# Optimization experiments

Measured on AMD Instinct MI355X. Metric: run time of the kernel, lower is better.

The kernel has to match this reference:

```python
import jax, jax.numpy as jnp
import numpy as np
from jax import lax

V, E, F, TL, NS, B = 10000, 150, 200, 7, 4, 2048
PAD_IDX = 1
EPS = 1e-5
SLOPE = 0.01  # nn.LeakyReLU default


def leaky(x):
    return jnp.where(x >= 0, x, SLOPE * x)


def conv1d(x, w, b):
    # x [B,Cin,L], w [Cout,Cin,K] -> [B,Cout,L-K+1]
    y = lax.conv_general_dilated(x, w, (1,), 'VALID',
                                 dimension_numbers=('NCH', 'OIH', 'NCH'))
    return y + b[None, :, None]


def batchnorm(x, g, b):
    # training-mode BatchNorm1d over [B,C,L]: stats over (B,L), biased var
    m = jnp.mean(x, axis=(0, 2), keepdims=True)
    v = jnp.mean((x - m) ** 2, axis=(0, 2), keepdims=True)
    return (x - m) * lax.rsqrt(v + EPS) * g[None, :, None] + b[None, :, None]


def setup_inputs() -> dict:
    key = jax.random.key(0)
    ks = jax.random.split(key, 24)
    s = 0.05
    inp = {
        'text': jax.random.randint(ks[0], (NS * TL, B), 0, V, dtype=jnp.int32).astype(jnp.int64) if False else jax.random.randint(ks[0], (NS * TL, B), 0, V),
        'ith_sentence': 4,
        'idx': 1,
        'emb': jax.random.normal(ks[1], (V, E), jnp.float32) * s,
        'gamma': jnp.ones((F,), jnp.float32),
        'beta': jnp.zeros((F,), jnp.float32),
        'conv1_w': jax.random.normal(ks[2], (F, E, 2), jnp.float32) * s,
        'conv1_b': jax.random.normal(ks[3], (F,), jnp.float32) * s,
        'conv2_w': jax.random.normal(ks[4], (F, F, 2), jnp.float32) * s,
        'conv2_b': jax.random.normal(ks[5], (F,), jnp.float32) * s,
        'conv3_w': jax.random.normal(ks[6], (F, F, 3), jnp.float32) * s,
        'conv3_b': jax.random.normal(ks[7], (F,), jnp.float32) * s,
        'conv4_w': jax.random.normal(ks[8], (F, F, 3), jnp.float32) * s,
        'conv4_b': jax.random.normal(ks[9], (F,), jnp.float32) * s,
        'M_w': jax.random.normal(ks[10], (F, 2 * F), jnp.float32) * s,
        'M_b': jax.random.normal(ks[11], (F,), jnp.float32) * s,
        'U_w': jax.random.normal(ks[12], (7, F, F), jnp.float32) * s,
        'U_b': jax.random.normal(ks[13], (7, F), jnp.float32) * s,
        'R_w': jax.random.normal(ks[14], (F, F), jnp.float32) * s,
        'R_b': jax.random.normal(ks[15], (F,), jnp.float32) * s,
        'H_w': jax.random.normal(ks[16], (F, F), jnp.float32) * s,
        'H_b': jax.random.normal(ks[17], (F,), jnp.float32) * s,
        'X_w': jax.random.normal(ks[18], (F, V), jnp.float32) * s,
        'X_b': jax.random.normal(ks[19], (F,), jnp.float32) * s,
        'Y_w': jax.random.normal(ks[20], (V, F), jnp.float32) * s,
        'Y_b': jax.random.normal(ks[21], (V,), jnp.float32) * s,
    }
    return inp


def _forward(text, ith_sentence, emb, gamma, beta,
             conv1_w, conv1_b, conv2_w, conv2_b, conv3_w, conv3_b,
             conv4_w, conv4_b, M_w, M_b, U_w, U_b, R_w, R_b,
             H_w, H_b, X_w, X_b, Y_w, Y_b):
    batch = text.shape[1]
    embedded = jnp.transpose(emb[text], (1, 2, 0))  # [B,E,S]

    # conv encoder per preceding sentence (Python loop over fixed small count)
    vecs = []
    for j in range(1, ith_sentence):
        seg = embedded[:, :, (j - 1) * TL: j * TL]        # [B,E,7]
        o = leaky(batchnorm(conv1d(seg, conv1_w, conv1_b), gamma, beta))  # L=6
        o = leaky(batchnorm(conv1d(o, conv2_w, conv2_b), gamma, beta))    # L=5
        o = leaky(batchnorm(conv1d(o, conv3_w, conv3_b), gamma, beta))    # L=3
        o = leaky(conv1d(o, conv4_w, conv4_b))                            # L=1
        vecs.append(o[:, :, 0])                           # [B,F]

    h = jnp.zeros((batch, F), embedded.dtype)
    for i in range(ith_sentence - 1):
        h = leaky(jnp.concatenate([vecs[i], h], axis=1) @ M_w.T + M_b)

    # u vectors; faithfully reproduce the original's u1-overwrite in the
    # text_len==7 branch: u1 becomes relu(U7(h)); u6,u7 stay un-activated.
    Uh = jnp.einsum('bf,tgf->tbg', h, U_w) + U_b[:, None, :]  # [7,B,F]
    Ur = leaky(Uh)
    u_steps = jnp.stack([Ur[6], Ur[1], Ur[2], Ur[3], Ur[4], Uh[5], Uh[6]])

    h_terms = jnp.einsum('tbf,gf->tbg', u_steps, H_w) + H_b   # [7,B,F]
    targets = lax.dynamic_slice_in_dim(text, (ith_sentence - 1) * TL, TL, 0)  # [7,B]

    XwT = X_w.T  # [V,F]; X(onehot(w)) == XwT[w] + X_b (same math, direct gather)

    def step(carry, xs):
        r, w = carry
        h_term, tgt = xs
        r = leaky(r @ R_w.T + R_b + XwT[w] + X_b + h_term)    # [B,F]
        y = r @ Y_w.T + Y_b                                   # [B,V]
        logp = jax.nn.log_softmax(y, axis=-1)
        loss_t = -jnp.mean(jnp.take_along_axis(logp, tgt[:, None], 1)[:, 0])
        pred = jnp.argmax(y, axis=1)
        correct_t = jnp.sum((pred == tgt).astype(jnp.int32))
        return (r, pred), (loss_t, correct_t)

    w0 = jnp.zeros((batch,), targets.dtype)
    r0 = jnp.zeros((batch, F), h.dtype)
    _, (losses, corrects) = lax.scan(step, (r0, w0), (h_terms, targets))
    return jnp.sum(losses), jnp.sum(corrects)


def reference(text, ith_sentence, idx, emb, gamma, beta,
              conv1_w, conv1_b, conv2_w, conv2_b, conv3_w, conv3_b,
              conv4_w, conv4_b, M_w, M_b, U_w, U_b, R_w, R_b,
              H_w, H_b, X_w, X_b, Y_w, Y_b):
    loss, correct = _forward(text, int(ith_sentence), emb, gamma, beta,
                             conv1_w, conv1_b, conv2_w, conv2_b,
                             conv3_w, conv3_b, conv4_w, conv4_b,
                             M_w, M_b, U_w, U_b, R_w, R_b,
                             H_w, H_b, X_w, X_b, Y_w, Y_b)
    return loss, correct
```

## Files before the change

### kernel.cpp

```cpp
#include <hip/hip_runtime.h>
#include <math.h>

#define V_    10000
#define VP_   10048
#define E_    150
#define F_    200
#define TL_   7
#define B_    2048
#define NSEG_ 3
#define EPS_  1e-5f
#define SLOPE_ 0.01f
#define NB64  (B_/64)
#define NVB   157
#define NYB   1280
#define KQ_   7

typedef unsigned short u16;
typedef __attribute__((ext_vector_type(8))) short bf16x8;
typedef __attribute__((ext_vector_type(4))) float f32x4;

#define SB0() __builtin_amdgcn_sched_barrier(0)

__device__ __forceinline__ float leaky_f(float x){ return x >= 0.f ? x : SLOPE_*x; }
__device__ __forceinline__ u16 bf16_rne(float x){
  unsigned u = __float_as_uint(x);
  unsigned r = (u + 0x7FFFu + ((u>>16)&1u)) >> 16;
  return (u16)r;
}
__device__ __forceinline__ float bf16_to_f(u16 h){ return __uint_as_float(((unsigned)h)<<16); }

__global__ void transpose_k(const float* __restrict__ in, float* __restrict__ out,
                            int R, int C)
{
  __shared__ float tile[32][33];
  const long long bofs = (long long)blockIdx.z * R * C;
  in += bofs; out += bofs;
  const int c0 = blockIdx.x*32, r0 = blockIdx.y*32;
  const int tx = threadIdx.x, ty = threadIdx.y;
  for (int i = ty; i < 32; i += 8) {
    int r = r0 + i, c = c0 + tx;
    if (r < R && c < C) tile[i][tx] = in[(long long)r*C + c];
  }
  __syncthreads();
  for (int i = ty; i < 32; i += 8) {
    int c = c0 + i, r = r0 + tx;
    if (c < C && r < R) out[(long long)c*R + r] = tile[tx][i];
  }
}

__global__ void gather_x0(const int* __restrict__ text, const float* __restrict__ emb,
                          float* __restrict__ X0)
{
  const int b = blockIdx.x*256 + threadIdx.x;
  const int l = blockIdx.y, j = blockIdx.z;
  const int s = j*TL_ + l;
  const int row = text[(long long)s*B_ + b];
  const float* er = emb + (long long)row*E_;
  float* xp = X0 + ((long long)j*E_*TL_ + l)*B_ + b;
  for (int e = 0; e < E_; ++e) xp[(long long)e*TL_*B_] = er[e];
}

struct PWEnt { const float* src; u16* dh; u16* dl; int kstride; int keff; int nq; };
struct PWTab { PWEnt e[14]; };

__global__ void pack_all_w(PWTab tab)
{
  const PWEnt E = tab.e[blockIdx.y];
  const int q = blockIdx.x;
  if (q >= E.nq) return;
  const int f = threadIdx.x;
  union { u16 u[32]; uint4 v[4]; } H, L;
  #pragma unroll
  for (int kk = 0; kk < 32; ++kk) {
    const int k = q*32 + kk;
    const float x = (k < E.keff && f < F_) ? E.src[(size_t)f*E.kstride + k] : 0.f;
    const u16 h = bf16_rne(x);
    H.u[kk] = h;
    L.u[kk] = bf16_rne(x - bf16_to_f(h));
  }
  uint4* dh = (uint4*)(E.dh + ((size_t)q*256 + f)*32);
  uint4* dl = (uint4*)(E.dl + ((size_t)q*256 + f)*32);
  #pragma unroll
  for (int i = 0; i < 4; ++i) { dh[i] = H.v[i]; dl[i] = L.v[i]; }
}

__global__ void pack_x(const float* __restrict__ X, long long xZ,
                       u16* __restrict__ Oh, u16* __restrict__ Ol, long long oZ)
{
  const int q = blockIdx.y, z = blockIdx.z;
  const int b = blockIdx.x*256 + threadIdx.x;
  X  += (size_t)z*xZ;
  Oh += (size_t)z*oZ; Ol += (size_t)z*oZ;
  union { u16 u[32]; uint4 v[4]; } H, L;
  #pragma unroll
  for (int kk = 0; kk < 32; ++kk) {
    const int k = q*32 + kk;
    const float x = (k < F_) ? X[(size_t)k*B_ + b] : 0.f;
    const u16 h = bf16_rne(x);
    H.u[kk] = h;
    L.u[kk] = bf16_rne(x - bf16_to_f(h));
  }
  uint4* dh = (uint4*)(Oh + ((size_t)q*B_ + b)*32);
  uint4* dl = (uint4*)(Ol + ((size_t)q*B_ + b)*32);
  #pragma unroll
  for (int i = 0; i < 4; ++i) { dh[i] = H.v[i]; dl[i] = L.v[i]; }
}

__global__ void us_pack(const float* __restrict__ Uh,
                        u16* __restrict__ Oh, u16* __restrict__ Ol, long long oZ)
{
  const int q = blockIdx.y, t = blockIdx.z;
  const int b = blockIdx.x*256 + threadIdx.x;
  const int src = (t == 0) ? 6 : t;
  const float* U = Uh + (size_t)src*F_*B_;
  Oh += (size_t)t*oZ; Ol += (size_t)t*oZ;
  union { u16 u[32]; uint4 v[4]; } H, L;
  #pragma unroll
  for (int kk = 0; kk < 32; ++kk) {
    const int k = q*32 + kk;
    float x = 0.f;
    if (k < F_) {
      x = U[(size_t)k*B_ + b];
      if (t < 5) x = leaky_f(x);
    }
    const u16 h = bf16_rne(x);
    H.u[kk] = h;
    L.u[kk] = bf16_rne(x - bf16_to_f(h));
  }
  uint4* dh = (uint4*)(Oh + ((size_t)q*B_ + b)*32);
  uint4* dl = (uint4*)(Ol + ((size_t)q*B_ + b)*32);
  #pragma unroll
  for (int i = 0; i < 4; ++i) { dh[i] = H.v[i]; dl[i] = L.v[i]; }
}

struct MFrag { bf16x8 h1[4], l1[4], h2[4], l2[4]; };

template<bool TWO>
__device__ __forceinline__ void m_loadq(MFrag& f, int q,
    const u16* __restrict__ X1h, const u16* __restrict__ X1l,
    const u16* __restrict__ X2h, const u16* __restrict__ X2l,
    int b0, int lr, int g)
{
  #pragma unroll
  for (int nt = 0; nt < 4; ++nt) {
    const size_t o = ((size_t)q*B_ + (b0 + nt*16 + lr))*32 + g*8;
    f.h1[nt] = *(const bf16x8*)(X1h + o);
    f.l1[nt] = *(const bf16x8*)(X1l + o);
    if (TWO) {
      f.h2[nt] = *(const bf16x8*)(X2h + o);
      f.l2[nt] = *(const bf16x8*)(X2l + o);
    }
  }
}

template<bool TWO>
__device__ __forceinline__ void m_mfma_chunk(const MFrag& f, int q,
    const u16* __restrict__ W1h, const u16* __restrict__ W1l,
    const u16* __restrict__ W2h, const u16* __restrict__ W2l,
    int f0, int w, int lr, int g, f32x4 acc[4])
{
  const size_t aoff = ((size_t)q*256 + (f0 + w*16 + lr))*32 + g*8;
  {
    const bf16x8 ah = *(const bf16x8*)(W1h + aoff);
    const bf16x8 al = *(const bf16x8*)(W1l + aoff);
    #pragma unroll
    for (int nt = 0; nt < 4; ++nt) {
      acc[nt] = __builtin_amdgcn_mfma_f32_16x16x32_bf16(ah, f.h1[nt], acc[nt], 0, 0, 0);
      acc[nt] = __builtin_amdgcn_mfma_f32_16x16x32_bf16(ah, f.l1[nt], acc[nt], 0, 0, 0);
      acc[nt] = __builtin_amdgcn_mfma_f32_16x16x32_bf16(al, f.h1[nt], acc[nt], 0, 0, 0);
    }
  }
  if (TWO) {
    const bf16x8 ah = *(const bf16x8*)(W2h + aoff);
    const bf16x8 al = *(const bf16x8*)(W2l + aoff);
    #pragma unroll
    for (int nt = 0; nt < 4; ++nt) {
      acc[nt] = __builtin_amdgcn_mfma_f32_16x16x32_bf16(ah, f.h2[nt], acc[nt], 0, 0, 0);
      acc[nt] = __builtin_amdgcn_mfma_f32_16x16x32_bf16(ah, f.l2[nt], acc[nt], 0, 0, 0);
      acc[nt] = __builtin_amdgcn_mfma_f32_16x16x32_bf16(al, f.h2[nt], acc[nt], 0, 0, 0);
    }
  }
}

template<bool TWO, bool LEAKY, bool OUT_F32, bool OUT_PK>
__global__ __launch_bounds__(256) void mf_gemm(
    const u16* __restrict__ W1h, const u16* __restrict__ W1l, long long wZ,
    const u16* __restrict__ X1h, const u16* __restrict__ X1l, long long xZ,
    const u16* __restrict__ W2h, const u16* __restrict__ W2l,
    const u16* __restrict__ X2h, const u16* __restrict__ X2l,
    const float* __restrict__ bias, long long bZ,
    float* __restrict__ Cf, long long cZ,
    u16* __restrict__ Oh, u16* __restrict__ Ol)
{
  const int z = blockIdx.z;
  W1h += (size_t)z*wZ; W1l += (size_t)z*wZ;
  X1h += (size_t)z*xZ; X1l += (size_t)z*xZ;
  const float* bz = bias + (size_t)z*bZ;
  if (OUT_F32) Cf += (size_t)z*cZ;

  const int f0 = blockIdx.x*64;
  const int b0 = blockIdx.y*64;
  const int tid = threadIdx.x;
  const int w = tid >> 6, l = tid & 63;
  const int lr = l & 15, g = l >> 4;

  __shared__ float T[64][65];

  f32x4 acc[4] = {};
  MFrag fA, fB;
  m_loadq<TWO>(fA, 0, X1h, X1l, X2h, X2l, b0, lr, g);
  #pragma unroll
  for (int q = 0; q < KQ_; ++q) {
    MFrag& cur = (q & 1) ? fB : fA;
    MFrag& nxt = (q & 1) ? fA : fB;
    if (q + 1 < KQ_) m_loadq<TWO>(nxt, q + 1, X1h, X1l, X2h, X2l, b0, lr, g);
    SB0();
    m_mfma_chunk<TWO>(cur, q, W1h, W1l, W2h, W2l, f0, w, lr, g, acc);
    SB0();
  }
  #pragma unroll
  for (int nt = 0; nt < 4; ++nt)
    #pragma unroll
    for (int j = 0; j < 4; ++j)
      T[w*16 + g*4 + j][nt*16 + lr] = acc[nt][j];
  __syncthreads();

  const int ty = tid >> 4, tx = tid & 15;
  #pragma unroll
  for (int i = 0; i < 4; ++i) {
    const int f = f0 + ty*4 + i;
    if (f < F_) {
      const float bb = bz[f];
      #pragma unroll
      for (int j = 0; j < 4; ++j) {
        float v = T[ty*4 + i][tx*4 + j] + bb;
        if (LEAKY) v = leaky_f(v);
        if (OUT_F32) Cf[(size_t)f*B_ + b0 + tx*4 + j] = v;
        T[ty*4 + i][tx*4 + j] = v;
      }
    } else {
      #pragma unroll
      for (int j = 0; j < 4; ++j) T[ty*4 + i][tx*4 + j] = 0.f;
    }
  }
  __syncthreads();

  if (OUT_PK) {
    const int bcol = tid & 63;
    const int kk0 = (tid >> 6)*8;
    #pragma unroll
    for (int qh = 0; qh < 2; ++qh) {
      const int q = (f0 >> 5) + qh;
      if (q >= KQ_) continue;
      union { u16 u[8]; uint4 v2[1]; } H, L;
      #pragma unroll
      for (int u = 0; u < 8; ++u) {
        const float x = T[qh*32 + kk0 + u][bcol];
        const u16 h = bf16_rne(x);
        H.u[u] = h;
        L.u[u] = bf16_rne(x - bf16_to_f(h));
      }
      const size_t off = ((size_t)q*B_ + b0 + bcol)*32 + kk0;
      *(uint4*)(Oh + off) = H.v2[0];
      *(uint4*)(Ol + off) = L.v2[0];
    }
  }
}

struct CFrag { bf16x8 bh[4], bl[4]; };

__device__ __forceinline__ void c_mfma_chunk(const CFrag& f, int q,
    const u16* __restrict__ Wh, const u16* __restrict__ Wl,
    int w, int lr, int g, f32x4 acc[4][4])
{
  bf16x8 ah[4], al[4];
  #pragma unroll
  for (int mt = 0; mt < 4; ++mt) {
    const size_t woff = ((size_t)q*256 + (w*64 + mt*16 + lr))*32 + g*8;
    ah[mt] = *(const bf16x8*)(Wh + woff);
    al[mt] = *(const bf16x8*)(Wl + woff);
  }
  #pragma unroll
  for (int mt = 0; mt < 4; ++mt)
    #pragma unroll
    for (int nt = 0; nt < 4; ++nt) {
      acc[mt][nt] = __builtin_amdgcn_mfma_f32_16x16x32_bf16(ah[mt], f.bh[nt], acc[mt][nt], 0, 0, 0);
      acc[mt][nt] = __builtin_amdgcn_mfma_f32_16x16x32_bf16(ah[mt], f.bl[nt], acc[mt][nt], 0, 0, 0);
      acc[mt][nt] = __builtin_amdgcn_mfma_f32_16x16x32_bf16(al[mt], f.bh[nt], acc[mt][nt], 0, 0, 0);
    }
}

template<int KW, int LIN, int NQ, int KEFF, bool BN>
__device__ __forceinline__ void c2_build(CFrag& f, int q,
    const float* __restrict__ Y, const float* __restrict__ bs_, const float* __restrict__ bh_,
    const int nbase[4], int g)
{
  const int kb = q*32 + g*8;
  int e  = kb / KW;
  int kw = kb - e*KW;
  #pragma unroll
  for (int u = 0; u < 8; ++u) {
    const int  li = e*LIN + kw;
    const bool ok = (kb + u) < KEFF;
    float sc = 0.f, sh = 0.f;
    if (BN && ok) { sc = bs_[e]; sh = bh_[e]; }
    #pragma unroll
    for (int nt = 0; nt < 4; ++nt) {
      float x = ok ? Y[(size_t)li*B_ + nbase[nt]] : 0.f;
      if (BN && ok) x = leaky_f(fmaf(x, sc, sh));
      const u16 h = bf16_rne(x);
      f.bh[nt][u] = (short)h;
      f.bl[nt][u] = (short)bf16_rne(x - bf16_to_f(h));
    }
    ++kw; if (kw == KW) { kw = 0; ++e; }
  }
}

template<int KW, int LIN, int NQ, int KEFF, bool BN, bool OUT_LEAKY>
__global__ __launch_bounds__(256, 2) void conv_gemm2(
    const u16* __restrict__ Wh, const u16* __restrict__ Wl,
    const float* __restrict__ Y, long long yZ,
    const float* __restrict__ bnS, const float* __restrict__ bnH,
    const float* __restrict__ bias, float* __restrict__ C, long long cZ, int Lout)
{
  const int z = blockIdx.y;
  Y += (size_t)z*yZ; C += (size_t)z*cZ;
  const float* bs_ = BN ? bnS + (size_t)z*F_ : nullptr;
  const float* bh_ = BN ? bnH + (size_t)z*F_ : nullptr;

  const int c0 = blockIdx.x*64;
  const int w  = threadIdx.x >> 6;
  const int l  = threadIdx.x & 63;
  const int lr = l & 15, g = l >> 4;

  int nbase[4];
  #pragma unroll
  for (int nt = 0; nt < 4; ++nt) {
    const int col = c0 + nt*16 + lr;
    nbase[nt] = (col >> 11)*B_ + (col & 2047);
  }

  f32x4 acc[4][4] = {};

  CFrag fA, fB;
  c2_build<KW,LIN,NQ,KEFF,BN>(fA, 0, Y, bs_, bh_, nbase, g);
  #pragma unroll
  for (int q = 0; q < NQ; ++q) {
    CFrag& cur = (q & 1) ? fB : fA;
    CFrag& nxt = (q & 1) ? fA : fB;
    if (q + 1 < NQ) c2_build<KW,LIN,NQ,KEFF,BN>(nxt, q + 1, Y, bs_, bh_, nbase, g);
    SB0();
    c_mfma_chunk(cur, q, Wh, Wl, w, lr, g, acc);
    SB0();
  }

  #pragma unroll
  for (int mt = 0; mt < 4; ++mt)
    #pragma unroll
    for (int j = 0; j < 4; ++j) {
      const int f = w*64 + mt*16 + g*4 + j;
      if (f < F_) {
        const float bs = bias[f];
        #pragma unroll
        for (int nt = 0; nt < 4; ++nt) {
          const int col = c0 + nt*16 + lr;
          const int t = col >> 11, b = col & 2047;
          float v = acc[mt][nt][j] + bs;
          if (OUT_LEAKY) v = leaky_f(v);
          C[((size_t)f*Lout + t)*B_ + b] = v;
        }
      }
    }
}

__global__ void bn_stats(const float* __restrict__ Y, int L,
                         const float* __restrict__ gamma, const float* __restrict__ beta,
                         float* __restrict__ scale, float* __restrict__ shift)
{
  const int f = blockIdx.x, j = blockIdx.y;
  const float* p = Y + ((long long)(j*F_ + f))*L*B_;
  const int N = L*B_;
  double s = 0.0, s2 = 0.0;
  for (int i = threadIdx.x; i < N; i += 256) { double x = p[i]; s += x; s2 += x*x; }
  __shared__ double sh1[256], sh2[256];
  sh1[threadIdx.x] = s; sh2[threadIdx.x] = s2;
  __syncthreads();
  for (int off = 128; off; off >>= 1) {
    if (threadIdx.x < off) { sh1[threadIdx.x] += sh1[threadIdx.x+off]; sh2[threadIdx.x] += sh2[threadIdx.x+off]; }
    __syncthreads();
  }
  if (threadIdx.x == 0) {
    const double mean = sh1[0]/N;
    const double var  = sh2[0]/N - mean*mean;
    const float rstd = rsqrtf((float)var + EPS_);
    const float sc = gamma[f]*rstd;
    scale[j*F_+f] = sc;
    shift[j*F_+f] = beta[f] - (float)mean*sc;
  }
}

struct RFrag { bf16x8 h[4], lo[4]; };

__device__ __forceinline__ void r_loadq(RFrag& f, int q,
    const u16* __restrict__ Ah, const u16* __restrict__ Al,
    int b0, int lr, int g)
{
  #pragma unroll
  for (int nt = 0; nt < 4; ++nt) {
    const size_t o = ((size_t)q*B_ + (b0 + nt*16 + lr))*32 + g*8;
    f.h[nt]  = *(const bf16x8*)(Ah + o);
    f.lo[nt] = *(const bf16x8*)(Al + o);
  }
}

__global__ __launch_bounds__(256) void r_step(
    const u16* __restrict__ RWh, const u16* __restrict__ RWl,
    const u16* __restrict__ Ain_h, const u16* __restrict__ Ain_l,
    const float* __restrict__ Rb, const float* __restrict__ XwT,
    const float* __restrict__ Xb, const float* __restrict__ HTt,
    const float4* __restrict__ pm4, const float* __restrict__ rPrev,
    const float* __restrict__ Yw, const float* __restrict__ YbF,
    const int* __restrict__ tgt_prev, float* __restrict__ loss_prev,
    int* __restrict__ corr_prev, int have_prev,
    float* __restrict__ rn, u16* __restrict__ Ahi, u16* __restrict__ Alo)
{
  const int f0 = blockIdx.x*64;
  const int b0 = blockIdx.y*64;
  const int tid = threadIdx.x;
  const int w = tid >> 6, l = tid & 63;
  const int lr = l & 15, g = l >> 4;

  __shared__ float T[64][65];
  __shared__ int w_sm[64];

  if (have_prev) {
    const int rr = l >> 2;
    const int ql = l & 3;
    const int row = b0 + w*16 + rr;
    float M = -INFINITY, S = 0.f; int ai = 0x7fffffff;
    for (int p = ql; p < NVB; p += 4) {
      const float4 qq = pm4[(size_t)p*B_ + row];
      const float mm = qq.x, ss = qq.y;
      const int idx = __float_as_int(qq.z);
      if (mm > M) ai = idx;
      else if (mm == M && idx < ai) ai = idx;
      const float M2 = fmaxf(M, mm);
      const float t1 = (M == -INFINITY) ? 0.f : S*__expf(M - M2);
      S = t1 + ss*__expf(mm - M2);
      M = M2;
    }
    const int tb = tgt_prev[row];
    float td = 0.f;
    for (int f2 = ql; f2 < F_; f2 += 4)
      td = fmaf(rPrev[(size_t)f2*B_ + row], Yw[(size_t)tb*F_ + f2], td);
    #pragma unroll
    for (int off = 1; off <= 2; off <<= 1) {
      td += __shfl_xor(td, off);
      const float om = __shfl_xor(M, off);
      const float os = __shfl_xor(S, off);
      const int   oai = __shfl_xor(ai, off);
      if (om > M) ai = oai;
      else if (om == M && oai < ai) ai = oai;
      const float M2 = fmaxf(M, om);
      const float t1 = (M  == -INFINITY) ? 0.f : S *__expf(M  - M2);
      const float t2 = (om == -INFINITY) ? 0.f : os*__expf(om - M2);
      S = t1 + t2;
      M = M2;
    }
    if (ql == 0) {
      if (blockIdx.x == 0) {
        loss_prev[row] = (M + logf(S)) - (td + YbF[tb]);
        corr_prev[row] = (ai == tb) ? 1 : 0;
      }
      w_sm[w*16 + rr] = ai;
    }
  } else {
    if (l < 16) w_sm[w*16 + l] = 0;
  }

  f32x4 acc[4] = {};
  RFrag fA, fB;
  r_loadq(fA, 0, Ain_h, Ain_l, b0, lr, g);
  #pragma unroll
  for (int q = 0; q < KQ_; ++q) {
    RFrag& cur = (q & 1) ? fB : fA;
    RFrag& nxt = (q & 1) ? fA : fB;
    if (q + 1 < KQ_) r_loadq(nxt, q + 1, Ain_h, Ain_l, b0, lr, g);
    SB0();
    {
      const size_t aoff = ((size_t)q*256 + (f0 + w*16 + lr))*32 + g*8;
      const bf16x8 ah = *(const bf16x8*)(RWh + aoff);
      const bf16x8 al = *(const bf16x8*)(RWl + aoff);
      #pragma unroll
      for (int nt = 0; nt < 4; ++nt) {
        acc[nt] = __builtin_amdgcn_mfma_f32_16x16x32_bf16(ah, cur.h[nt],  acc[nt], 0, 0, 0);
        acc[nt] = __builtin_amdgcn_mfma_f32_16x16x32_bf16(ah, cur.lo[nt], acc[nt], 0, 0, 0);
        acc[nt] = __builtin_amdgcn_mfma_f32_16x16x32_bf16(al, cur.h[nt],  acc[nt], 0, 0, 0);
      }
    }
    SB0();
  }
  #pragma unroll
  for (int nt = 0; nt < 4; ++nt)
    #pragma unroll
    for (int j = 0; j < 4; ++j)
      T[w*16 + g*4 + j][nt*16 + lr] = acc[nt][j];
  __syncthreads();

  const int ty = tid >> 4, tx = tid & 15;
  int wv[4];
  #pragma unroll
  for (int j = 0; j < 4; ++j) {
    int t_ = w_sm[tx*4 + j];
    wv[j] = (t_ < 0) ? 0 : (t_ >= V_ ? V_-1 : t_);
  }

  #pragma unroll
  for (int i = 0; i < 4; ++i) {
    const int f = f0 + ty*4 + i;
    if (f < F_) {
      const float rb = Rb[f] + Xb[f];
      #pragma unroll
      for (int j = 0; j < 4; ++j) {
        const int b = b0 + tx*4 + j;
        float v = T[ty*4 + i][tx*4 + j] + rb + XwT[(size_t)wv[j]*F_ + f] + HTt[(size_t)f*B_ + b];
        v = leaky_f(v);
        rn[(size_t)f*B_ + b] = v;
        T[ty*4 + i][tx*4 + j] = v;
      }
    } else {
      #pragma unroll
      for (int j = 0; j < 4; ++j) T[ty*4 + i][tx*4 + j] = 0.f;
    }
  }
  __syncthreads();

  const int bcol = tid & 63;
  const int kk0 = (tid >> 6)*8;
  #pragma unroll
  for (int qh = 0; qh < 2; ++qh) {
    const int q = (f0 >> 5) + qh;
    if (q >= KQ_) continue;
    union { u16 u[8]; uint4 v2[1]; } H, L;
    #pragma unroll
    for (int u = 0; u < 8; ++u) {
      const float x = T[qh*32 + kk0 + u][bcol];
      const u16 h = bf16_rne(x);
      H.u[u] = h;
      L.u[u] = bf16_rne(x - bf16_to_f(h));
    }
    const size_t off = ((size_t)q*B_ + b0 + bcol)*32 + kk0;
    *(uint4*)(Ahi + off) = H.v2[0];
    *(uint4*)(Alo + off) = L.v2[0];
  }
}

__global__ void pack_yw(const float* __restrict__ Yw, const float* __restrict__ Yb,
                        u16* __restrict__ Bhi, u16* __restrict__ Blo, float* __restrict__ YbP)
{
  const int q = blockIdx.x;
  const int v = blockIdx.y*256 + threadIdx.x;
  if (v >= VP_) return;
  if (q == 0) YbP[v] = (v < V_) ? Yb[v] : -INFINITY;
  union { u16 u[32]; uint4 w[4]; } H, L;
  #pragma unroll
  for (int kk = 0; kk < 32; ++kk) {
    const int f = q*32 + kk;
    const float x = (f < F_ && v < V_) ? Yw[(size_t)v*F_ + f] : 0.f;
    const u16 h = bf16_rne(x);
    H.u[kk] = h;
    L.u[kk] = bf16_rne(x - bf16_to_f(h));
  }
  uint4* dh = (uint4*)(Bhi + ((size_t)q*VP_ + v)*32);
  uint4* dl = (uint4*)(Blo + ((size_t)q*VP_ + v)*32);
  #pragma unroll
  for (int i = 0; i < 4; ++i) { dh[i] = H.w[i]; dl[i] = L.w[i]; }
}

struct YFrag2 { bf16x8 ah[4], al[4], bh[4], bl[4]; };

__device__ __forceinline__ void y_loadq2(YFrag2& f, int q,
    const u16* __restrict__ Ahi, const u16* __restrict__ Alo,
    const u16* __restrict__ Bhi, const u16* __restrict__ Blo,
    int b0, int v0, int w, int lr, int g)
{
  #pragma unroll
  for (int mt = 0; mt < 4; ++mt) {
    const size_t o = ((size_t)q*B_ + (b0 + w*64 + mt*16 + lr))*32 + g*8;
    f.ah[mt] = *(const bf16x8*)(Ahi + o);
    f.al[mt] = *(const bf16x8*)(Alo + o);
  }
  #pragma unroll
  for (int nt = 0; nt < 4; ++nt) {
    const size_t o = ((size_t)q*VP_ + (v0 + nt*16 + lr))*32 + g*8;
    f.bh[nt] = *(const bf16x8*)(Bhi + o);
    f.bl[nt] = *(const bf16x8*)(Blo + o);
  }
}

__device__ __forceinline__ void y_mfmaq2(const YFrag2& f, f32x4 acc[4][4])
{
  #pragma unroll
  for (int mt = 0; mt < 4; ++mt)
    #pragma unroll
    for (int nt = 0; nt < 4; ++nt) {
      acc[mt][nt] = __builtin_amdgcn_mfma_f32_16x16x32_bf16(f.ah[mt], f.bh[nt], acc[mt][nt], 0, 0, 0);
      acc[mt][nt] = __builtin_amdgcn_mfma_f32_16x16x32_bf16(f.ah[mt], f.bl[nt], acc[mt][nt], 0, 0, 0);
      acc[mt][nt] = __builtin_amdgcn_mfma_f32_16x16x32_bf16(f.al[mt], f.bh[nt], acc[mt][nt], 0, 0, 0);
    }
}

__global__ __launch_bounds__(256, 2) void y_mfma(
    const u16* __restrict__ Ahi, const u16* __restrict__ Alo,
    const u16* __restrict__ Bhi, const u16* __restrict__ Blo,
    const float* __restrict__ YbP, float4* __restrict__ pm4)
{
  const int bid = blockIdx.x;
  const int xcd = bid & 7;
  const int i   = bid >> 3;
  const int by  = i & 7;
  const int vb  = xcd*20 + (i >> 3);
  if (vb >= NVB) return;
  const int v0 = vb*64;
  const int b0 = by*256;
  const int w  = threadIdx.x >> 6;
  const int l  = threadIdx.x & 63;
  const int lr = l & 15;
  const int g  = l >> 4;

  f32x4 acc[4][4] = {};

  YFrag2 fA, fB;
  y_loadq2(fA, 0, Ahi, Alo, Bhi, Blo, b0, v0, w, lr, g);
  #pragma unroll
  for (int q = 0; q < KQ_; ++q) {
    YFrag2& cur = (q & 1) ? fB : fA;
    YFrag2& nxt = (q & 1) ? fA : fB;
    if (q + 1 < KQ_)
      y_loadq2(nxt, q + 1, Ahi, Alo, Bhi, Blo, b0, v0, w, lr, g);
    SB0();
    __builtin_amdgcn_s_setprio(1);
    y_mfmaq2(cur, acc);
    __builtin_amdgcn_s_setprio(0);
    SB0();
  }

  float ybv[4];
  #pragma unroll
  for (int nt = 0; nt < 4; ++nt) ybv[nt] = YbP[v0 + nt*16 + lr];

  float m[4][4]; int ai[4][4];
  #pragma unroll
  for (int mt = 0; mt < 4; ++mt)
    #pragma unroll
    for (int j = 0; j < 4; ++j) { m[mt][j] = -INFINITY; ai[mt][j] = 0x7fffffff; }

  #pragma unroll
  for (int nt = 0; nt < 4; ++nt) {
    const int colv = v0 + nt*16 + lr;
    #pragma unroll
    for (int mt = 0; mt < 4; ++mt)
      #pragma unroll
      for (int j = 0; j < 4; ++j) {
        const float y = acc[mt][nt][j] + ybv[nt];
        if (y > m[mt][j]) { m[mt][j] = y; ai[mt][j] = colv; }
      }
  }
  #pragma unroll
  for (int off = 1; off <= 8; off <<= 1) {
    #pragma unroll
    for (int mt = 0; mt < 4; ++mt)
      #pragma unroll
      for (int j = 0; j < 4; ++j) {
        const float om = __shfl_xor(m[mt][j], off);
        const int   oai = __shfl_xor(ai[mt][j], off);
        if (om > m[mt][j] || (om == m[mt][j] && oai < ai[mt][j])) { m[mt][j] = om; ai[mt][j] = oai; }
      }
  }

  float s[4][4] = {};
  #pragma unroll
  for (int nt = 0; nt < 4; ++nt) {
    #pragma unroll
    for (int mt = 0; mt < 4; ++mt)
      #pragma unroll
      for (int j = 0; j < 4; ++j)
        s[mt][j] += __expf(acc[mt][nt][j] + ybv[nt] - m[mt][j]);
  }
  #pragma unroll
  for (int off = 1; off <= 8; off <<= 1) {
    #pragma unroll
    for (int mt = 0; mt < 4; ++mt)
      #pragma unroll
      for (int j = 0; j < 4; ++j)
        s[mt][j] += __shfl_xor(s[mt][j], off);
  }

  if (lr == 0) {
    #pragma unroll
    for (int mt = 0; mt < 4; ++mt)
      #pragma unroll
      for (int j = 0; j < 4; ++j) {
        const int row = b0 + w*64 + mt*16 + g*4 + j;
        pm4[(size_t)vb*B_ + row] = make_float4(m[mt][j], s[mt][j], __int_as_float(ai[mt][j]), 0.f);
      }
  }
}

__global__ void combine2(const float4* __restrict__ pm4,
                         const float* __restrict__ r, const float* __restrict__ Yw,
                         const float* __restrict__ Yb, const int* __restrict__ tgt,
                         int* __restrict__ w, float* __restrict__ loss_row,
                         int* __restrict__ corr_row)
{
  const int b = blockIdx.x*4 + (threadIdx.x >> 6);
  const int lane = threadIdx.x & 63;
  const int tb = tgt[b];

  float td = 0.f;
  #pragma unroll
  for (int it = 0; it < 4; ++it) {
    const int f = lane + it*64;
    if (f < F_) td = fmaf(r[(size_t)f*B_ + b], Yw[(size_t)tb*F_ + f], td);
  }

  float M = -INFINITY, S = 0.f; int ai = 0x7fffffff;
  for (int p = lane; p < NVB; p += 64) {
    const float4 q = pm4[(size_t)p*B_ + b];
    const float mm = q.x, s = q.y;
    const int idx = __float_as_int(q.z);
    if (mm > M) ai = idx;
    else if (mm == M && idx < ai) ai = idx;
    const float M2 = fmaxf(M, mm);
    const float t1 = (M == -INFINITY) ? 0.f : S*__expf(M - M2);
    S = t1 + s*__expf(mm - M2);
    M = M2;
  }
  #pragma unroll
  for (int off = 1; off <= 32; off <<= 1) {
    td += __shfl_xor(td, off);
    const float om = __shfl_xor(M, off);
    const float os = __shfl_xor(S, off);
    const int   oai = __shfl_xor(ai, off);
    if (om > M) ai = oai;
    else if (om == M && oai < ai) ai = oai;
    const float M2 = fmaxf(M, om);
    const float t1 = (M  == -INFINITY) ? 0.f : S *__expf(M  - M2);
    const float t2 = (om == -INFINITY) ? 0.f : os*__expf(om - M2);
    S = t1 + t2;
    M = M2;
  }
  if (lane == 0) {
    const float logZ = M + logf(S);
    loss_row[b] = logZ - (td + Yb[tb]);
    corr_row[b] = (ai == tb) ? 1 : 0;
    w[b] = ai;
  }
}

__global__ void finalize_k(const float* __restrict__ lr, const int* __restrict__ cr,
                           float* __restrict__ out)
{
  __shared__ float sf[256]; __shared__ int si[256];
  float s = 0.f; int c = 0;
  for (int i = threadIdx.x; i < 7*B_; i += 256) { s += lr[i]; c += cr[i]; }
  sf[threadIdx.x] = s; si[threadIdx.x] = c;
  __syncthreads();
  for (int off = 128; off; off >>= 1) {
    if (threadIdx.x < off) { sf[threadIdx.x] += sf[threadIdx.x+off]; si[threadIdx.x] += si[threadIdx.x+off]; }
    __syncthreads();
  }
  if (threadIdx.x == 0) { out[0] = sf[0] / (float)B_; out[1] = (float)si[0]; }
}

extern "C" void kernel_launch(void* const* d_in, const int* in_sizes, int n_in,
                              void* d_out, int out_size, void* d_ws, size_t ws_size,
                              hipStream_t stream)
{
  (void)in_sizes; (void)n_in; (void)out_size; (void)ws_size;
  const int*   text = (const int*)d_in[0];
  const float* emb  = (const float*)d_in[3];
  const float* gamma= (const float*)d_in[4];
  const float* beta = (const float*)d_in[5];
  const float* c1w = (const float*)d_in[6];  const float* c1b = (const float*)d_in[7];
  const float* c2w = (const float*)d_in[8];  const float* c2b = (const float*)d_in[9];
  const float* c3w = (const float*)d_in[10]; const float* c3b = (const float*)d_in[11];
  const float* c4w = (const float*)d_in[12]; const float* c4b = (const float*)d_in[13];
  const float* Mw = (const float*)d_in[14];  const float* Mb = (const float*)d_in[15];
  const float* Uw = (const float*)d_in[16];  const float* Ub = (const float*)d_in[17];
  const float* Rw = (const float*)d_in[18];  const float* Rb = (const float*)d_in[19];
  const float* Hw = (const float*)d_in[20];  const float* Hb = (const float*)d_in[21];
  const float* Xw = (const float*)d_in[22];  const float* Xb = (const float*)d_in[23];
  const float* Yw = (const float*)d_in[24];  const float* Yb = (const float*)d_in[25];

  float* ws = (float*)d_ws;
  size_t off = 0;
  auto alloc = [&](size_t n)->float* { float* p = ws + off; off += (n + 63) & ~(size_t)63; return p; };

  u16* W1h = (u16*)alloc((size_t)10*256*32/2); u16* W1l = (u16*)alloc((size_t)10*256*32/2);
  u16* W2h = (u16*)alloc((size_t)13*256*32/2); u16* W2l = (u16*)alloc((size_t)13*256*32/2);
  u16* W3h = (u16*)alloc((size_t)19*256*32/2); u16* W3l = (u16*)alloc((size_t)19*256*32/2);
  u16* W4h = (u16*)alloc((size_t)19*256*32/2); u16* W4l = (u16*)alloc((size_t)19*256*32/2);
  u16* RWh = (u16*)alloc((size_t)7*256*32/2);  u16* RWl = (u16*)alloc((size_t)7*256*32/2);
  u16* MW1h= (u16*)alloc((size_t)7*256*32/2);  u16* MW1l= (u16*)alloc((size_t)7*256*32/2);
  u16* MW2h= (u16*)alloc((size_t)7*256*32/2);  u16* MW2l= (u16*)alloc((size_t)7*256*32/2);
  u16* UWh = (u16*)alloc((size_t)6*7*256*32/2);u16* UWl = (u16*)alloc((size_t)6*7*256*32/2);
  u16* HWh = (u16*)alloc((size_t)7*256*32/2);  u16* HWl = (u16*)alloc((size_t)7*256*32/2);
  float* S1 = alloc(3*F_); float* Sh1 = alloc(3*F_);
  float* S2 = alloc(3*F_); float* Sh2 = alloc(3*F_);
  float* S3 = alloc(3*F_); float* Sh3 = alloc(3*F_);
  float* YbP = alloc(VP_);
  float* P  = alloc((size_t)NSEG_*E_*TL_*B_);
  float* Q  = alloc((size_t)NSEG_*F_*6*B_);
  float* VEC = alloc((size_t)NSEG_*F_*B_);
  float* rA = alloc((size_t)F_*B_);
  float* rB = alloc((size_t)F_*B_);
  u16* PKh = (u16*)alloc((size_t)13*10240*32/2);
  u16* PKl = (u16*)alloc((size_t)13*10240*32/2);
  int*   wbuf = (int*)alloc(B_);
  float* loss_rows = alloc((size_t)7*B_);
  int*   corr_rows = (int*)alloc((size_t)7*B_);

  float* X0 = P;
  float* Y1 = Q;
  float* Y2 = P;
  float* Y3 = Q;
  float* Uh = Q;
  float* HT = P;

  const size_t HT_FL = (size_t)7*F_*B_;
  u16* YWhi = (u16*)(P + HT_FL);
  u16* YWlo = YWhi + (size_t)KQ_*VP_*32;
  u16* A0h  = YWlo + (size_t)KQ_*VP_*32;
  u16* A0l  = A0h + (size_t)KQ_*B_*32;
  u16* A1h  = A0l + (size_t)KQ_*B_*32;
  u16* A1l  = A1h + (size_t)KQ_*B_*32;

  u16* hAh = (u16*)(Q + (size_t)5734400);
  u16* hAl = hAh + (size_t)KQ_*B_*32;
  u16* hBh = hAl + (size_t)KQ_*B_*32;
  u16* hBl = hBh + (size_t)KQ_*B_*32;

  u16* VPh = PKh;  u16* VPl = PKl;
  u16* USh = PKh;  u16* USl = PKl;

  float4* pm4 = (float4*)Q;
  float*  XwT = Q + (size_t)2097152;

  const long long FRZ = (long long)KQ_*B_*32;
  const long long WQZ = (long long)KQ_*256*32;

  const dim3 tb_(32,8);

  PWTab tab;
  tab.e[0] = { c1w,      W1h,  W1l,  300, 300, 10 };
  tab.e[1] = { c2w,      W2h,  W2l,  400, 400, 13 };
  tab.e[2] = { c3w,      W3h,  W3l,  600, 600, 19 };
  tab.e[3] = { c4w,      W4h,  W4l,  600, 600, 19 };
  tab.e[4] = { Rw,       RWh,  RWl,  200, 200, 7 };
  tab.e[5] = { Mw,       MW1h, MW1l, 400, 200, 7 };
  tab.e[6] = { Mw + 200, MW2h, MW2l, 400, 200, 7 };
  tab.e[7] = { Hw,       HWh,  HWl,  200, 200, 7 };
  for (int i = 0; i < 6; ++i)
    tab.e[8+i] = { Uw + (size_t)(1+i)*F_*F_, UWh + (size_t)i*WQZ, UWl + (size_t)i*WQZ, 200, 200, 7 };
  hipLaunchKernelGGL(pack_all_w, dim3(19, 14), dim3(256), 0, stream, tab);

  hipLaunchKernelGGL(gather_x0, dim3(B_/256, TL_, NSEG_), dim3(256), 0, stream, text, emb, X0);

  hipLaunchKernelGGL((conv_gemm2<2,7,10,300,false,false>), dim3(192,3), dim3(256), 0, stream,
      W1h, W1l, X0, (long long)E_*TL_*B_, nullptr, nullptr, c1b, Y1, (long long)F_*6*B_, 6);
  hipLaunchKernelGGL(bn_stats, dim3(F_, NSEG_), dim3(256), 0, stream, Y1, 6, gamma, beta, S1, Sh1);
  hipLaunchKernelGGL((conv_gemm2<2,6,13,400,true,false>), dim3(160,3), dim3(256), 0, stream,
      W2h, W2l, Y1, (long long)F_*6*B_, S1, Sh1, c2b, Y2, (long long)F_*5*B_, 5);
  hipLaunchKernelGGL(bn_stats, dim3(F_, NSEG_), dim3(256), 0, stream, Y2, 5, gamma, beta, S2, Sh2);
  hipLaunchKernelGGL((conv_gemm2<3,5,19,600,true,false>), dim3(96,3), dim3(256), 0, stream,
      W3h, W3l, Y2, (long long)F_*5*B_, S2, Sh2, c3b, Y3, (long long)F_*3*B_, 3);
  hipLaunchKernelGGL(bn_stats, dim3(F_, NSEG_), dim3(256), 0, stream, Y3, 3, gamma, beta, S3, Sh3);
  hipLaunchKernelGGL((conv_gemm2<3,3,19,600,true,true>), dim3(32,3), dim3(256), 0, stream,
      W4h, W4l, Y3, (long long)F_*3*B_, S3, Sh3, c4b, VEC, (long long)F_*B_, 1);

  hipLaunchKernelGGL(pack_x, dim3(B_/256, KQ_, NSEG_), dim3(256), 0, stream,
      VEC, (long long)F_*B_, VPh, VPl, FRZ);
  hipMemsetAsync(hAh, 0, (size_t)2*KQ_*B_*32*2, stream);
  u16 *hch = hAh, *hcl = hAl, *hnh = hBh, *hnl = hBl;
  for (int i = 0; i < 3; ++i) {
    hipLaunchKernelGGL((mf_gemm<true,true,false,true>), dim3(4, 32, 1), dim3(256), 0, stream,
        MW1h, MW1l, 0, VPh + (size_t)i*FRZ, VPl + (size_t)i*FRZ, 0,
        MW2h, MW2l, hch, hcl, Mb, 0, nullptr, 0, hnh, hnl);
    u16* t1 = hch; hch = hnh; hnh = t1;
    u16* t2 = hcl; hcl = hnl; hnl = t2;
  }

  hipLaunchKernelGGL((mf_gemm<false,false,true,false>), dim3(4, 32, 6), dim3(256), 0, stream,
      UWh, UWl, WQZ, hch, hcl, 0, nullptr, nullptr, nullptr, nullptr,
      Ub + F_, F_, Uh + (size_t)F_*B_, (long long)F_*B_, nullptr, nullptr);
  hipLaunchKernelGGL(us_pack, dim3(B_/256, KQ_, 7), dim3(256), 0, stream,
      Uh, USh, USl, FRZ);
  hipLaunchKernelGGL((mf_gemm<false,false,true,false>), dim3(4, 32, 7), dim3(256), 0, stream,
      HWh, HWl, 0, USh, USl, FRZ, nullptr, nullptr, nullptr, nullptr,
      Hb, 0, HT, (long long)F_*B_, nullptr, nullptr);

  hipLaunchKernelGGL(transpose_k, dim3(313,7,1), tb_, 0, stream, Xw, XwT, F_, V_);
  hipLaunchKernelGGL(pack_yw, dim3(KQ_, (VP_+255)/256), dim3(256), 0, stream, Yw, Yb, YWhi, YWlo, YbP);
  hipMemsetAsync(A0h, 0, (size_t)2*KQ_*B_*32*2, stream);

  u16 *cin_h = A0h, *cin_l = A0l, *cout_h = A1h, *cout_l = A1l;
  float *rOld = rA, *rNew = rB;
  for (int t = 0; t < 7; ++t) {
    const int* tgt_prev = text + (size_t)(20 + t)*B_;
    float* lp = (t > 0) ? loss_rows + (size_t)(t-1)*B_ : loss_rows;
    int*   cp = (t > 0) ? corr_rows + (size_t)(t-1)*B_ : corr_rows;
    hipLaunchKernelGGL(r_step, dim3(4, 32), dim3(256), 0, stream,
        RWh, RWl, cin_h, cin_l, Rb, XwT, Xb, HT + (size_t)t*F_*B_,
        pm4, rOld, Yw, Yb, tgt_prev, lp, cp, (int)(t > 0),
        rNew, cout_h, cout_l);
    hipLaunchKernelGGL(y_mfma, dim3(NYB), dim3(256), 0, stream,
        cout_h, cout_l, YWhi, YWlo, YbP, pm4);
    float* tr = rOld; rOld = rNew; rNew = tr;
    u16* th = cin_h; cin_h = cout_h; cout_h = th;
    u16* tl = cin_l; cin_l = cout_l; cout_l = tl;
  }
  hipLaunchKernelGGL(combine2, dim3(B_/4), dim3(256), 0, stream,
      pm4, rOld, Yw, Yb, text + (size_t)27*B_, wbuf,
      loss_rows + (size_t)6*B_, corr_rows + (size_t)6*B_);

  hipLaunchKernelGGL(finalize_k, dim3(1), dim3(256), 0, stream, loss_rows, corr_rows, (float*)d_out);
}
```

Baseline: 1.065 ms.

## Stage conv im2col B-fragments through double-buffered LDS shared across warps

Until now each of the four warps built its own copy of the B fragments (im2col gather, BN+leaky, bf16 hi/lo split) straight from global memory, so the same work and loads were repeated four times. Now each thread builds one 8-element slice for the whole block, writes it into a double-buffered LDS tile, and the warps read their fragments from LDS. Global loads for the next chunk are issued before the MFMAs and converted afterwards. This cuts redundant global traffic and conversion work, at the cost of a __syncthreads per K-chunk, extra LDS use, and dropping the min-2-blocks launch bound.

Result: faster. 968.7 us (-9.0%).

```diff
diff --git a/kernel.cpp b/kernel.cpp
--- a/kernel.cpp
+++ b/kernel.cpp
@@ -267,57 +267,8 @@
   }
 }
 
-struct CFrag { bf16x8 bh[4], bl[4]; };
-
-__device__ __forceinline__ void c_mfma_chunk(const CFrag& f, int q,
-    const u16* __restrict__ Wh, const u16* __restrict__ Wl,
-    int w, int lr, int g, f32x4 acc[4][4])
-{
-  bf16x8 ah[4], al[4];
-  #pragma unroll
-  for (int mt = 0; mt < 4; ++mt) {
-    const size_t woff = ((size_t)q*256 + (w*64 + mt*16 + lr))*32 + g*8;
-    ah[mt] = *(const bf16x8*)(Wh + woff);
-    al[mt] = *(const bf16x8*)(Wl + woff);
-  }
-  #pragma unroll
-  for (int mt = 0; mt < 4; ++mt)
-    #pragma unroll
-    for (int nt = 0; nt < 4; ++nt) {
-      acc[mt][nt] = __builtin_amdgcn_mfma_f32_16x16x32_bf16(ah[mt], f.bh[nt], acc[mt][nt], 0, 0, 0);
-      acc[mt][nt] = __builtin_amdgcn_mfma_f32_16x16x32_bf16(ah[mt], f.bl[nt], acc[mt][nt], 0, 0, 0);
-      acc[mt][nt] = __builtin_amdgcn_mfma_f32_16x16x32_bf16(al[mt], f.bh[nt], acc[mt][nt], 0, 0, 0);
-    }
-}
-
-template<int KW, int LIN, int NQ, int KEFF, bool BN>
-__device__ __forceinline__ void c2_build(CFrag& f, int q,
-    const float* __restrict__ Y, const float* __restrict__ bs_, const float* __restrict__ bh_,
-    const int nbase[4], int g)
-{
-  const int kb = q*32 + g*8;
-  int e  = kb / KW;
-  int kw = kb - e*KW;
-  #pragma unroll
-  for (int u = 0; u < 8; ++u) {
-    const int  li = e*LIN + kw;
-    const bool ok = (kb + u) < KEFF;
-    float sc = 0.f, sh = 0.f;
-    if (BN && ok) { sc = bs_[e]; sh = bh_[e]; }
-    #pragma unroll
-    for (int nt = 0; nt < 4; ++nt) {
-      float x = ok ? Y[(size_t)li*B_ + nbase[nt]] : 0.f;
-      if (BN && ok) x = leaky_f(fmaf(x, sc, sh));
-      const u16 h = bf16_rne(x);
-      f.bh[nt][u] = (short)h;
-      f.bl[nt][u] = (short)bf16_rne(x - bf16_to_f(h));
-    }
-    ++kw; if (kw == KW) { kw = 0; ++e; }
-  }
-}
-
 template<int KW, int LIN, int NQ, int KEFF, bool BN, bool OUT_LEAKY>
-__global__ __launch_bounds__(256, 2) void conv_gemm2(
+__global__ __launch_bounds__(256) void conv_gemm3(
     const u16* __restrict__ Wh, const u16* __restrict__ Wl,
     const float* __restrict__ Y, long long yZ,
     const float* __restrict__ bnS, const float* __restrict__ bnH,
@@ -329,29 +280,100 @@
   const float* bh_ = BN ? bnH + (size_t)z*F_ : nullptr;
 
   const int c0 = blockIdx.x*64;
-  const int w  = threadIdx.x >> 6;
-  const int l  = threadIdx.x & 63;
+  const int tid = threadIdx.x;
+  const int w  = tid >> 6;
+  const int l  = tid & 63;
   const int lr = l & 15, g = l >> 4;
 
-  int nbase[4];
-  #pragma unroll
-  for (int nt = 0; nt < 4; ++nt) {
-    const int col = c0 + nt*16 + lr;
-    nbase[nt] = (col >> 11)*B_ + (col & 2047);
-  }
+  const int col_s = tid & 63;
+  const int ks    = (tid >> 6)*8;
+  const int cg    = c0 + col_s;
+  const int ts    = cg >> 11, bcol_s = cg & 2047;
+
+  __shared__ u16 LH[2][64][32];
+  __shared__ u16 LL[2][64][32];
 
   f32x4 acc[4][4] = {};
-
-  CFrag fA, fB;
-  c2_build<KW,LIN,NQ,KEFF,BN>(fA, 0, Y, bs_, bh_, nbase, g);
+  float rawA[8], rawB[8];
+
+  {
+    const int kb = ks;
+    int e = kb / KW, kw = kb - e*KW;
+    #pragma unroll
+    for (int u = 0; u < 8; ++u) {
+      rawA[u] = ((kb + u) < KEFF) ? Y[((size_t)(e*LIN + ts + kw))*B_ + bcol_s] : 0.f;
+      ++kw; if (kw == KW) { kw = 0; ++e; }
+    }
+    union { u16 u[8]; uint4 v; } Hh, Ll;
+    e = kb / KW; kw = kb - e*KW;
+    #pragma unroll
+    for (int u = 0; u < 8; ++u) {
+      float x = rawA[u];
+      if (BN && (kb + u) < KEFF) x = leaky_f(fmaf(x, bs_[e], bh_[e]));
+      const u16 h = bf16_rne(x);
+      Hh.u[u] = h; Ll.u[u] = bf16_rne(x - bf16_to_f(h));
+      ++kw; if (kw == KW) { kw = 0; ++e; }
+    }
+    *(uint4*)&LH[0][col_s][ks] = Hh.v;
+    *(uint4*)&LL[0][col_s][ks] = Ll.v;
+  }
+  __syncthreads();
+
   #pragma unroll
   for (int q = 0; q < NQ; ++q) {
-    CFrag& cur = (q & 1) ? fB : fA;
-    CFrag& nxt = (q & 1) ? fA : fB;
-    if (q + 1 < NQ) c2_build<KW,LIN,NQ,KEFF,BN>(nxt, q + 1, Y, bs_, bh_, nbase, g);
+    const int buf = q & 1;
+    float (&rw)[8] = (q & 1) ? rawA : rawB;
+
+    if (q + 1 < NQ) {
+      const int kb = (q + 1)*32 + ks;
+      int e = kb / KW, kw = kb - e*KW;
+      #pragma unroll
+      for (int u = 0; u < 8; ++u) {
+        rw[u] = ((kb + u) < KEFF) ? Y[((size_t)(e*LIN + ts + kw))*B_ + bcol_s] : 0.f;
+        ++kw; if (kw == KW) { kw = 0; ++e; }
+      }
+    }
     SB0();
-    c_mfma_chunk(cur, q, Wh, Wl, w, lr, g, acc);
+    {
+      bf16x8 bh4[4], bl4[4];
+      #pragma unroll
+      for (int nt = 0; nt < 4; ++nt) {
+        bh4[nt] = *(const bf16x8*)&LH[buf][nt*16 + lr][g*8];
+        bl4[nt] = *(const bf16x8*)&LL[buf][nt*16 + lr][g*8];
+      }
+      bf16x8 ah[4], al[4];
+      #pragma unroll
+      for (int mt = 0; mt < 4; ++mt) {
+        const size_t woff = ((size_t)q*256 + (w*64 + mt*16 + lr))*32 + g*8;
+        ah[mt] = *(const bf16x8*)(Wh + woff);
+        al[mt] = *(const bf16x8*)(Wl + woff);
+      }
+      #pragma unroll
+      for (int mt = 0; mt < 4; ++mt)
+        #pragma unroll
+        for (int nt = 0; nt < 4; ++nt) {
+          acc[mt][nt] = __builtin_amdgcn_mfma_f32_16x16x32_bf16(ah[mt], bh4[nt], acc[mt][nt], 0, 0, 0);
+          acc[mt][nt] = __builtin_amdgcn_mfma_f32_16x16x32_bf16(ah[mt], bl4[nt], acc[mt][nt], 0, 0, 0);
+          acc[mt][nt] = __builtin_amdgcn_mfma_f32_16x16x32_bf16(al[mt], bh4[nt], acc[mt][nt], 0, 0, 0);
+        }
+    }
     SB0();
+    if (q + 1 < NQ) {
+      const int kb = (q + 1)*32 + ks;
+      int e = kb / KW, kw = kb - e*KW;
+      union { u16 u[8]; uint4 v; } Hh, Ll;
+      #pragma unroll
+      for (int u = 0; u < 8; ++u) {
+        float x = rw[u];
+        if (BN && (kb + u) < KEFF) x = leaky_f(fmaf(x, bs_[e], bh_[e]));
+        const u16 h = bf16_rne(x);
+        Hh.u[u] = h; Ll.u[u] = bf16_rne(x - bf16_to_f(h));
+        ++kw; if (kw == KW) { kw = 0; ++e; }
+      }
+      *(uint4*)&LH[buf ^ 1][col_s][ks] = Hh.v;
+      *(uint4*)&LL[buf ^ 1][col_s][ks] = Ll.v;
+    }
+    __syncthreads();
   }
 
   #pragma unroll
@@ -867,16 +889,16 @@
 
   hipLaunchKernelGGL(gather_x0, dim3(B_/256, TL_, NSEG_), dim3(256), 0, stream, text, emb, X0);
 
-  hipLaunchKernelGGL((conv_gemm2<2,7,10,300,false,false>), dim3(192,3), dim3(256), 0, stream,
+  hipLaunchKernelGGL((conv_gemm3<2,7,10,300,false,false>), dim3(192,3), dim3(256), 0, stream,
       W1h, W1l, X0, (long long)E_*TL_*B_, nullptr, nullptr, c1b, Y1, (long long)F_*6*B_, 6);
   hipLaunchKernelGGL(bn_stats, dim3(F_, NSEG_), dim3(256), 0, stream, Y1, 6, gamma, beta, S1, Sh1);
-  hipLaunchKernelGGL((conv_gemm2<2,6,13,400,true,false>), dim3(160,3), dim3(256), 0, stream,
+  hipLaunchKernelGGL((conv_gemm3<2,6,13,400,true,false>), dim3(160,3), dim3(256), 0, stream,
       W2h, W2l, Y1, (long long)F_*6*B_, S1, Sh1, c2b, Y2, (long long)F_*5*B_, 5);
   hipLaunchKernelGGL(bn_stats, dim3(F_, NSEG_), dim3(256), 0, stream, Y2, 5, gamma, beta, S2, Sh2);
-  hipLaunchKernelGGL((conv_gemm2<3,5,19,600,true,false>), dim3(96,3), dim3(256), 0, stream,
+  hipLaunchKernelGGL((conv_gemm3<3,5,19,600,true,false>), dim3(96,3), dim3(256), 0, stream,
       W3h, W3l, Y2, (long long)F_*5*B_, S2, Sh2, c3b, Y3, (long long)F_*3*B_, 3);
   hipLaunchKernelGGL(bn_stats, dim3(F_, NSEG_), dim3(256), 0, stream, Y3, 3, gamma, beta, S3, Sh3);
-  hipLaunchKernelGGL((conv_gemm2<3,3,19,600,true,true>), dim3(32,3), dim3(256), 0, stream,
+  hipLaunchKernelGGL((conv_gemm3<3,3,19,600,true,true>), dim3(32,3), dim3(256), 0, stream,
       W4h, W4l, Y3, (long long)F_*3*B_, S3, Sh3, c4b, VEC, (long long)F_*B_, 1);
 
   hipLaunchKernelGGL(pack_x, dim3(B_/256, KQ_, NSEG_), dim3(256), 0, stream,
```
